# Kernel optimization log

Hardware: AMD Instinct MI355X
Metric: run time of the kernel (lower is better)

Reference implementation:

```python
import jax, jax.numpy as jnp
import numpy as np

N, T, D, C = 32, 512, 1024, 120
EPS = 1e-12
SCALE = 2.0 * (D ** 0.5)


def setup_inputs() -> dict:
    key = jax.random.key(0)
    ks = jax.random.split(key, 16)
    inp = {
        'anc_perm_input': jax.random.normal(ks[0], (N, T, D), dtype=jnp.float32),
        'pos_perm_input': jax.random.normal(ks[1], (N, T, D), dtype=jnp.float32),
        'neg_perm_input': jax.random.normal(ks[2], (N, T, D), dtype=jnp.float32),
        'anc_src_key_padding_mask': jax.random.randint(ks[3], (N, T), 0, 2) == 1,
        'pos_src_key_padding_mask': jax.random.randint(ks[4], (N, T), 0, 2) == 1,
        'neg_src_key_padding_mask': jax.random.randint(ks[5], (N, T), 0, 2) == 1,
        # learned parameters (stored as (in, out); math-equivalent to torch x @ W.T)
        'W_attn': jax.random.normal(ks[6], (D, D), dtype=jnp.float32) * 0.02,
        'b_attn': jnp.zeros((D,), dtype=jnp.float32),
        'W1': jax.random.normal(ks[7], (D, D), dtype=jnp.float32) * 0.02,
        'b1': jnp.zeros((D,), dtype=jnp.float32),
        'W2': jax.random.normal(ks[8], (D, D), dtype=jnp.float32) * 0.02,
        'b2': jnp.zeros((D,), dtype=jnp.float32),
        'ln_g': jnp.ones((D,), dtype=jnp.float32),
        'ln_b': jnp.zeros((D,), dtype=jnp.float32),
        'W_last': jax.random.normal(ks[9], (D, C), dtype=jnp.float32) * 0.02,
        'b_last': jnp.zeros((C,), dtype=jnp.float32),
    }
    return inp


def _ntd_nd(x, mask, W_attn, b_attn, W1, b1, W2, b2, ln_g, ln_b, W_last, b_last):
    # x: (N,T,D); mask: (N,T) bool, True = padding
    w = x @ W_attn + b_attn                                   # (N,T,D)
    valid = ~mask                                             # (N,T)
    scores = jnp.einsum('btd,bsd->bts', w, w)                 # (N,T,T)
    scores = jnp.where(valid[:, :, None] & valid[:, None, :], scores, 0.0)
    s = jnp.sum(scores, axis=1) / SCALE                       # (N,T)
    s = jnp.where(mask, -jnp.inf, s)
    attn = jax.nn.softmax(s, axis=1)                          # (N,T)
    # proj_head: duplicate OrderedDict key => linear1 -> relu -> linear2 (no final act)
    proj = jax.nn.relu(x @ W1 + b1) @ W2 + b2                 # (N,T,D)
    pooled = jnp.einsum('bt,btd->bd', attn, proj)             # (N,D)
    mu = jnp.mean(pooled, axis=-1, keepdims=True)
    var = jnp.var(pooled, axis=-1, keepdims=True)
    normed = (pooled - mu) / jnp.sqrt(var + EPS) * ln_g + ln_b
    return jax.nn.relu(normed) @ W_last + b_last              # (N,C)


def reference(anc_perm_input, pos_perm_input, neg_perm_input,
              anc_src_key_padding_mask, pos_src_key_padding_mask, neg_src_key_padding_mask,
              W_attn, b_attn, W1, b1, W2, b2, ln_g, ln_b, W_last, b_last):
    params = (W_attn, b_attn, W1, b1, W2, b2, ln_g, ln_b, W_last, b_last)
    anc = _ntd_nd(anc_perm_input, anc_src_key_padding_mask, *params)
    pos = _ntd_nd(pos_perm_input, pos_src_key_padding_mask, *params)
    neg = _ntd_nd(neg_perm_input, neg_src_key_padding_mask, *params)
    return (anc, pos, neg)
```

## Files before the change

kernel.cpp:

```cpp
#include <hip/hip_runtime.h>
#include <hip/hip_bf16.h>
#include <math.h>

#define N_B 32
#define T_S 512
#define D_D 1024
#define C_C 120
#define ZB 96
#define SCALE 64.0f

typedef unsigned short u16;
typedef __attribute__((ext_vector_type(8))) short short8;
typedef __attribute__((ext_vector_type(8))) unsigned short ushort8;
typedef __attribute__((ext_vector_type(4))) float floatx4;

__device__ inline u16 f2bf(float f) {
    union { __hip_bfloat16 h; u16 u; } c; c.h = __float2bfloat16(f); return c.u;
}
__device__ inline float bf2f(u16 u) {
    union { unsigned i; float f; } c; c.i = ((unsigned)u) << 16; return c.f;
}

__device__ inline void gll16(const void* g, void* l) {
    __builtin_amdgcn_global_load_lds((const __attribute__((address_space(1))) void*)g,
                                     (__attribute__((address_space(3))) void*)l,
                                     16, 0, 0);
}

__device__ inline bool mask_is_i8(const int* mk) {
    bool i8 = false;
#pragma unroll
    for (int i = 0; i < 16; i++) {
        unsigned v = ((const unsigned*)mk)[i];
        if (v > 1u) i8 = true;
    }
    return i8;
}
__device__ inline int mask_val(const int* mk, int idx, bool i8) {
    return i8 ? (int)((const signed char*)mk)[idx] : mk[idx];
}

__global__ __launch_bounds__(512)
void k_scan(const int* m0, const int* m1, const int* m2,
            int* __restrict__ slotbase, int* __restrict__ cnts,
            int* __restrict__ gb, int* __restrict__ zblk,
            int* __restrict__ mtot, u16* __restrict__ xp,
            float* __restrict__ attnw, float4* __restrict__ zreg) {
    int zb = blockIdx.x;
    int tid = threadIdx.x;
    {
        float4 zz4 = {0.f, 0.f, 0.f, 0.f};
        for (int i = zb * 512 + tid; i < (2 * 1024 * 1024 / 16); i += ZB * 512)
            zreg[i] = zz4;
    }
    bool i8_0 = mask_is_i8(m0), i8_1 = mask_is_i8(m1), i8_2 = mask_is_i8(m2);
    __shared__ unsigned short wc[ZB][8];
    __shared__ int scnt[ZB], sgb[ZB], stot;
    int wave = tid >> 6, lane = tid & 63;
#pragma unroll
    for (int it = 0; it < 12; it++) {
        int zb2 = wave * 12 + it;
        int z2 = zb2 >> 5, b2 = zb2 & 31;
        const int* mk = z2 == 0 ? m0 : (z2 == 1 ? m1 : m2);
        bool i8 = z2 == 0 ? i8_0 : (z2 == 1 ? i8_1 : i8_2);
        int c = 0;
        if (i8) {
            const signed char* p = (const signed char*)mk + b2 * T_S + lane * 8;
#pragma unroll
            for (int e = 0; e < 8; e++) c += (p[e] == 0);
        } else {
            const int* p = mk + b2 * T_S + lane * 8;
#pragma unroll
            for (int e = 0; e < 8; e++) c += (p[e] == 0);
        }
        c += __shfl_xor(c, 1, 64);
        c += __shfl_xor(c, 2, 64);
        c += __shfl_xor(c, 4, 64);
        if ((lane & 7) == 0) wc[zb2][lane >> 3] = (unsigned short)c;
    }
    __syncthreads();
    if (tid < ZB) {
        int s = 0;
#pragma unroll
        for (int c = 0; c < 8; c++) s += wc[tid][c];
        scnt[tid] = s;
    }
    __syncthreads();
    if (tid == 0) {
        int run = 0;
        for (int i = 0; i < ZB; i++) { sgb[i] = run; run += (scnt[i] + 63) & ~63; }
        stot = run;
    }
    __syncthreads();
    int cnt = scnt[zb], base = sgb[zb];
    if (tid == 0) {
        cnts[zb] = cnt; gb[zb] = base;
        int run = base;
#pragma unroll
        for (int c = 0; c < 8; c++) { slotbase[zb * 8 + c] = run; run += wc[zb][c]; }
        if (zb == ZB - 1) mtot[0] = stot;
    }
    int nb = (cnt + 63) >> 6;
    if (tid < nb) zblk[(base >> 6) + tid] = zb;
    int cend = (cnt + 63) & ~63;
    {
        u16* bp = xp + (size_t)(base + cnt) * D_D;
        int n8 = (cend - cnt) * (D_D / 8);
        ushort8 zz = {0,0,0,0,0,0,0,0};
        for (int i = tid; i < n8; i += 512)
            *(ushort8*)(bp + (size_t)i * 8) = zz;
    }
    if (zb == ZB - 1) {
        int tot = stot, tend = (tot + 255) & ~255;
        u16* bp = xp + (size_t)tot * D_D;
        int n8 = (tend - tot) * (D_D / 8);
        ushort8 zz = {0,0,0,0,0,0,0,0};
        for (int i = tid; i < n8; i += 512)
            *(ushort8*)(bp + (size_t)i * 8) = zz;
        for (int i = tid; i < tend - tot; i += 512) attnw[tot + i] = 0.f;
        if (tid < ((tend - tot) >> 6)) zblk[(tot >> 6) + tid] = 0;
    }
}

__global__ void k_prep(const float* __restrict__ W_attn, const float* __restrict__ W1,
                       const float* x0, const float* x1, const float* x2,
                       const int* m0, const int* m1, const int* m2,
                       const int* __restrict__ slotbase,
                       float* __restrict__ WT, u16* __restrict__ W1T,
                       float* __restrict__ xsum, u16* __restrict__ xp) {
    int bx = blockIdx.x;
    int tid = threadIdx.x;
    if (bx < 1024) {
        int tbx = bx & 31, tby = bx >> 5;
        __shared__ float tile[32][33];
        int tx = tid & 31, ty = tid >> 5;
#pragma unroll
        for (int j = 0; j < 32; j += 8)
            tile[ty + j][tx] = W_attn[(size_t)(tby*32 + ty + j)*D_D + tbx*32 + tx];
        __syncthreads();
#pragma unroll
        for (int j = 0; j < 32; j += 8)
            WT[(size_t)(tbx*32 + ty + j)*D_D + tby*32 + tx] = tile[tx][ty + j];
        __syncthreads();
#pragma unroll
        for (int j = 0; j < 32; j += 8)
            tile[ty + j][tx] = W1[(size_t)(tby*32 + ty + j)*D_D + tbx*32 + tx];
        __syncthreads();
#pragma unroll
        for (int j = 0; j < 32; j += 8)
            W1T[(size_t)(tbx*32 + ty + j)*D_D + tby*32 + tx] = f2bf(tile[tx][ty + j]);
        return;
    }
    int idx = bx - 1024;
    int chunk = idx & 7, zb = idx >> 3;
    int z = zb >> 5, b = zb & 31;
    const float* x = z == 0 ? x0 : (z == 1 ? x1 : x2);
    const int* mk = z == 0 ? m0 : (z == 1 ? m1 : m2);
    bool i8 = mask_is_i8(mk);
    int t0 = chunk * 64;
    __shared__ unsigned char s_list[64];
    __shared__ int s_cc;
    if (tid < 64) {
        bool v = (mask_val(mk, b * T_S + t0 + tid, i8) == 0);
        unsigned long long bal = __ballot(v);
        int pos = (int)__popcll(bal & ((1ull << tid) - 1ull));
        if (v) s_list[pos] = (unsigned char)tid;
        if (tid == 0) s_cc = (int)__popcll(bal);
    }
    __syncthreads();
    int cc = s_cc;
    int slot0 = slotbase[zb * 8 + chunk];
    const float4* xr = (const float4*)(x + (size_t)(b * T_S) * D_D);
    float4 acc = {0.f, 0.f, 0.f, 0.f};
#pragma unroll 4
    for (int j = 0; j < cc; j++) {
        int t = t0 + (int)s_list[j];
        float4 v = xr[(size_t)t * 256 + tid];
        union { __hip_bfloat162 h; ushort2 u; } c0, c1;
        c0.h = __float22bfloat162_rn({v.x, v.y});
        c1.h = __float22bfloat162_rn({v.z, v.w});
        ushort4 uu = {c0.u.x, c0.u.y, c1.u.x, c1.u.y};
        *(ushort4*)(xp + (size_t)(slot0 + j) * D_D + tid * 4) = uu;
        acc.x += v.x; acc.y += v.y; acc.z += v.z; acc.w += v.w;
    }
    float* xs = xsum + (size_t)zb * D_D + tid * 4;
    atomicAdd(xs + 0, acc.x); atomicAdd(xs + 1, acc.y);
    atomicAdd(xs + 2, acc.z); atomicAdd(xs + 3, acc.w);
}

__global__ void k_matvec(const float* __restrict__ W, const float* __restrict__ vin,
                         const float* __restrict__ bias, const int* __restrict__ bmul,
                         float scale, float* __restrict__ vout) {
    int z = blockIdx.z, bg = blockIdx.y;
    int och = blockIdx.x >> 3, kc = blockIdx.x & 7;
    int o = och * 256 + threadIdx.x;
    int brow = z * N_B + bg * 8;
    float acc[8] = {0.f, 0.f, 0.f, 0.f, 0.f, 0.f, 0.f, 0.f};
    if (kc == 0 && bias) {
        float bv = bias[o];
#pragma unroll
        for (int bb = 0; bb < 8; bb++)
            acc[bb] = bmul ? bv * (float)bmul[brow + bb] : bv;
    }
    const float* vi = vin + (size_t)brow * D_D + kc * 128;
    const float* Wp = W + (size_t)(kc * 128) * D_D + o;
#pragma unroll 4
    for (int i = 0; i < 128; i++) {
        float wv = Wp[(size_t)i * D_D];
#pragma unroll
        for (int bb = 0; bb < 8; bb++)
            acc[bb] += vi[(size_t)bb * D_D + i] * wv;
    }
#pragma unroll
    for (int bb = 0; bb < 8; bb++)
        atomicAdd(&vout[(size_t)(brow + bb) * D_D + o], acc[bb] * scale);
}

__global__ void k_dots(const u16* __restrict__ xp, const float* __restrict__ vs,
                       const int* __restrict__ zblk, const int* __restrict__ mtot,
                       float* __restrict__ sdot) {
    int t0 = blockIdx.x * 4;
    if (t0 >= mtot[0]) return;
    int t = t0 + (threadIdx.x >> 6);
    int lane = threadIdx.x & 63;
    int zb = zblk[t0 >> 6];
    const u16* xr = xp + (size_t)t * D_D;
    const float* vr = vs + (size_t)zb * D_D;
    float acc = 0.f;
#pragma unroll
    for (int i = 0; i < 2; i++) {
        short8 v = *(const short8*)(xr + i * 512 + lane * 8);
        const float* vp = vr + i * 512 + lane * 8;
        float4 a0 = *(const float4*)(vp);
        float4 a1 = *(const float4*)(vp + 4);
        acc += bf2f((u16)v[0]) * a0.x + bf2f((u16)v[1]) * a0.y
             + bf2f((u16)v[2]) * a0.z + bf2f((u16)v[3]) * a0.w
             + bf2f((u16)v[4]) * a1.x + bf2f((u16)v[5]) * a1.y
             + bf2f((u16)v[6]) * a1.z + bf2f((u16)v[7]) * a1.w;
    }
#pragma unroll
    for (int off = 32; off; off >>= 1) acc += __shfl_xor(acc, off, 64);
    if (lane == 0) sdot[t] = acc;
}

__global__ void k_smax(const float* __restrict__ sdot, const int* __restrict__ cnts,
                       const int* __restrict__ gb, float* __restrict__ attnw) {
    int zb = blockIdx.x, tid = threadIdx.x;
    __shared__ float redm[8], reds[8];
    int cnt = cnts[zb], base = gb[zb];
    int wave = tid >> 6, lane = tid & 63;
    float v = (tid < cnt) ? sdot[base + tid] : -INFINITY;
    float mx = v;
#pragma unroll
    for (int off = 32; off; off >>= 1) mx = fmaxf(mx, __shfl_xor(mx, off, 64));
    if (lane == 0) redm[wave] = mx;
    __syncthreads();
    mx = redm[0];
#pragma unroll
    for (int k = 1; k < 8; k++) mx = fmaxf(mx, redm[k]);
    float e = __expf(v - mx);
    float es = e;
#pragma unroll
    for (int off = 32; off; off >>= 1) es += __shfl_xor(es, off, 64);
    if (lane == 0) reds[wave] = es;
    __syncthreads();
    float tot = 0.f;
#pragma unroll
    for (int k = 0; k < 8; k++) tot += reds[k];
    int cend = (cnt + 63) & ~63;
    if (tid < cend) attnw[base + tid] = (tid < cnt) ? (e / tot) : 0.f;
}

#define STAGE_TILE(buf, k0)                                                   \
    {                                                                         \
        _Pragma("unroll")                                                     \
        for (int i_ = 0; i_ < 4; i_++) {                                      \
            int r0_ = i_ * 64 + wave * 8;                                     \
            int rr_ = r0_ + srow;                                             \
            int gc_ = cp ^ srow;            \
            gll16(abase + (size_t)rr_ * D_D + (k0) + gc_ * 8,                 \
                  &As[buf][r0_ * 64]);                                        \
            gll16(bbase + (size_t)rr_ * D_D + (k0) + gc_ * 8,                 \
                  &Bs[buf][r0_ * 64]);                                        \
        }                                                                     \
    }

__global__ __launch_bounds__(512, 1)
void k_gemm_bf16(const u16* __restrict__ xp, const u16* __restrict__ W1T,
                 const float* __restrict__ b1, const float* __restrict__ attnw,
                 const int* __restrict__ zblk, const int* __restrict__ mtot,
                 float* __restrict__ rbuf) {
    int bid = blockIdx.x;
    int sub = bid & 31;
    int Mt = (bid >> 5) * 8 + (sub & 7);
    int Nt = sub >> 3;
    int row0 = Mt * 256, N0 = Nt * 256;
    if (row0 >= mtot[0]) return;

    __shared__ __align__(16) u16 As[2][256 * 64];
    __shared__ __align__(16) u16 Bs[2][256 * 64];
    __shared__ float sAttn[256];
    int tid = threadIdx.x;
    int wave = tid >> 6, lane = tid & 63;
    if (tid < 256) sAttn[tid] = attnw[row0 + tid];

    int wy = wave >> 2, wx = wave & 3;
    int q = lane >> 4, cidx = lane & 15;
    int srow = lane >> 3;
    int cp = lane & 7;

    floatx4 acc[8][4];
#pragma unroll
    for (int mi = 0; mi < 8; mi++)
#pragma unroll
        for (int ni = 0; ni < 4; ni++)
            acc[mi][ni] = (floatx4){0.f, 0.f, 0.f, 0.f};

    const u16* abase = xp + (size_t)row0 * D_D;
    const u16* bbase = W1T + (size_t)N0 * D_D;

    STAGE_TILE(0, 0)
    __syncthreads();
    int cur = 0;
#pragma unroll 2
    for (int kt = 0; kt < 16; kt++) {
        if (kt < 15) { STAGE_TILE(cur ^ 1, (kt + 1) << 6) }
        __builtin_amdgcn_sched_barrier(0);
#pragma unroll
        for (int ks = 0; ks < 2; ks++) {
            short8 a[8], bfr[4];
#pragma unroll
            for (int mi = 0; mi < 8; mi++) {
                int m = wy * 128 + mi * 16 + cidx;
                a[mi] = *(const short8*)&As[cur][m * 64 + ((((ks << 2) | q) ^ (m & 7)) << 3)];
            }
#pragma unroll
            for (int ni = 0; ni < 4; ni++) {
                int n = wx * 64 + ni * 16 + cidx;
                bfr[ni] = *(const short8*)&Bs[cur][n * 64 + ((((ks << 2) | q) ^ (n & 7)) << 3)];
            }
#pragma unroll
            for (int mi = 0; mi < 8; mi++)
#pragma unroll
                for (int ni = 0; ni < 4; ni++)
                    acc[mi][ni] = __builtin_amdgcn_mfma_f32_16x16x32_bf16(
                        a[mi], bfr[ni], acc[mi][ni], 0, 0, 0);
        }
        __syncthreads();
        cur ^= 1;
    }

    int zb0 = zblk[(row0 >> 6) + wy * 2];
    int zb1 = zblk[(row0 >> 6) + wy * 2 + 1];
#pragma unroll
    for (int ni = 0; ni < 4; ni++) {
        int ng = N0 + wx * 64 + ni * 16 + cidx;
        float b1v = b1[ng];
        float s0 = 0.f, s1 = 0.f;
#pragma unroll
        for (int mi = 0; mi < 8; mi++) {
            float part = 0.f;
#pragma unroll
            for (int rg = 0; rg < 4; rg++) {
                int ml = wy * 128 + mi * 16 + q * 4 + rg;
                float hv = fmaxf(acc[mi][ni][rg] + b1v, 0.f);
                part += hv * sAttn[ml];
            }
            if (mi < 4) s0 += part; else s1 += part;
        }
        s0 += __shfl_xor(s0, 16, 64); s0 += __shfl_xor(s0, 32, 64);
        s1 += __shfl_xor(s1, 16, 64); s1 += __shfl_xor(s1, 32, 64);
        if (lane < 16) {
            atomicAdd(&rbuf[(size_t)zb0 * D_D + ng], s0);
            atomicAdd(&rbuf[(size_t)zb1 * D_D + ng], s1);
        }
    }
}

__global__ void k_fin(const float* __restrict__ pooled, const float* __restrict__ ln_g,
                      const float* __restrict__ ln_b, const float* __restrict__ Wl,
                      const float* __restrict__ bl, float* __restrict__ out) {
    int zb = blockIdx.x;
    int tid = threadIdx.x;
    __shared__ float nr[D_D];
    __shared__ float redA[8], redB[8];
    __shared__ float ps[4][C_C];
    const float* p = pooled + (size_t)zb * D_D;
    int o0 = tid, o1 = tid + 512;
    float a0 = p[o0], a1 = p[o1];
    float s1 = a0 + a1, s2 = a0 * a0 + a1 * a1;
#pragma unroll
    for (int off = 32; off; off >>= 1) {
        s1 += __shfl_xor(s1, off, 64);
        s2 += __shfl_xor(s2, off, 64);
    }
    int w = tid >> 6;
    if ((tid & 63) == 0) { redA[w] = s1; redB[w] = s2; }
    __syncthreads();
    float t1 = 0.f, t2 = 0.f;
#pragma unroll
    for (int k = 0; k < 8; k++) { t1 += redA[k]; t2 += redB[k]; }
    float mu = t1 * (1.0f / D_D);
    float var = t2 * (1.0f / D_D) - mu * mu;
    float rstd = 1.0f / sqrtf(var + 1e-12f);
    nr[o0] = fmaxf((a0 - mu) * rstd * ln_g[o0] + ln_b[o0], 0.f);
    nr[o1] = fmaxf((a1 - mu) * rstd * ln_g[o1] + ln_b[o1], 0.f);
    __syncthreads();
    if (tid < 4 * C_C) {
        int seg = tid / C_C, c = tid - seg * C_C;
        const float* wp = Wl + (size_t)(seg * 256) * C_C + c;
        const float* np = nr + seg * 256;
        float acc = 0.f;
#pragma unroll 8
        for (int d = 0; d < 256; d++)
            acc += np[d] * wp[(size_t)d * C_C];
        ps[seg][c] = acc;
    }
    __syncthreads();
    if (tid < C_C)
        out[(size_t)zb * C_C + tid] =
            bl[tid] + ps[0][tid] + ps[1][tid] + ps[2][tid] + ps[3][tid];
}

extern "C" void kernel_launch(void* const* d_in, const int* in_sizes, int n_in,
                              void* d_out, int out_size, void* d_ws, size_t ws_size,
                              hipStream_t stream) {
    const float* x0 = (const float*)d_in[0];
    const float* x1 = (const float*)d_in[1];
    const float* x2 = (const float*)d_in[2];
    const int* m0 = (const int*)d_in[3];
    const int* m1 = (const int*)d_in[4];
    const int* m2 = (const int*)d_in[5];
    const float* W_attn = (const float*)d_in[6];
    const float* b_attn = (const float*)d_in[7];
    const float* W1 = (const float*)d_in[8];
    const float* b1 = (const float*)d_in[9];
    const float* W2 = (const float*)d_in[10];
    const float* b2 = (const float*)d_in[11];
    const float* ln_g = (const float*)d_in[12];
    const float* ln_b = (const float*)d_in[13];
    const float* W_last = (const float*)d_in[14];
    const float* b_last = (const float*)d_in[15];
    float* out = (float*)d_out;

    char* wsb = (char*)d_ws;
    const size_t MB = 1 << 20;
    float* WT     = (float*)(wsb);
    u16*   W1T    = (u16*)  (wsb + 4 * MB);
    float* xsum   = (float*)(wsb + 6 * MB);
    float* rbuf   = (float*)(wsb + 6 * MB + 393216);
    float* wsum   = (float*)(wsb + 6 * MB + 786432);
    float* vs     = (float*)(wsb + 6 * MB + 1179648);
    float* pooled = (float*)(wsb + 6 * MB + 1572864);
    float* sdot   = (float*)(wsb + 8 * MB);
    float* attnw  = (float*)(wsb + 8 * MB + 262144);
    int*   slotb  = (int*)  (wsb + 8 * MB + 524288);
    int*   cnts   = (int*)  (wsb + 8 * MB + 528384);
    int*   gb     = (int*)  (wsb + 8 * MB + 532480);
    int*   mtot   = (int*)  (wsb + 8 * MB + 536576);
    int*   zblk   = (int*)  (wsb + 8 * MB + 540672);
    u16*   xp     = (u16*)  (wsb + 9 * MB);

    k_scan  <<<ZB, 512, 0, stream>>>(m0, m1, m2, slotb, cnts, gb, zblk, mtot,
                                     xp, attnw, (float4*)(wsb + 6 * MB));
    k_prep  <<<1792, 256, 0, stream>>>(W_attn, W1, x0, x1, x2, m0, m1, m2,
                                       slotb, WT, W1T, xsum, xp);
    k_matvec<<<dim3(32, 4, 3), 256, 0, stream>>>(W_attn, xsum, b_attn, cnts, 1.0f, wsum);
    k_matvec<<<dim3(32, 4, 3), 256, 0, stream>>>(WT, wsum, nullptr, nullptr, 1.0f / SCALE, vs);
    k_dots  <<<12288, 256, 0, stream>>>(xp, vs, zblk, mtot, sdot);
    k_smax  <<<ZB, 512, 0, stream>>>(sdot, cnts, gb, attnw);
    k_gemm_bf16<<<768, 512, 0, stream>>>(xp, W1T, b1, attnw, zblk, mtot, rbuf);
    k_matvec<<<dim3(32, 4, 3), 256, 0, stream>>>(W2, rbuf, b2, nullptr, 1.0f, pooled);
    k_fin   <<<ZB, 512, 0, stream>>>(pooled, ln_g, ln_b, W_last, b_last, out);
}
```

Measured before the change: 373.3 us.

## Fuse softmax into GEMM prologue and weight transposes into scan kernel

Removes the separate softmax kernel: each GEMM block recomputes the per-sequence max and sum from the dot scores for the sequences its 256 rows touch, then builds its attention weights in shared memory. Moves the W_attn/W1 transpose blocks from the prep kernel into the scan kernel, which now launches 1024 extra blocks, so the prep kernel only packs x. This cuts two kernel launches' worth of serialization and the attnw round trip. In exchange every GEMM block repeats softmax reductions with extra barriers, and padded tail rows now depend on zblk and sdot values instead of explicitly zeroed attnw.

```diff
diff --git a/kernel.cpp b/kernel.cpp
--- a/kernel.cpp
+++ b/kernel.cpp
@@ -42,12 +42,36 @@
 
 __global__ __launch_bounds__(512)
 void k_scan(const int* m0, const int* m1, const int* m2,
+            const float* __restrict__ W_attn, const float* __restrict__ W1,
             int* __restrict__ slotbase, int* __restrict__ cnts,
             int* __restrict__ gb, int* __restrict__ zblk,
             int* __restrict__ mtot, u16* __restrict__ xp,
-            float* __restrict__ attnw, float4* __restrict__ zreg) {
+            float* __restrict__ WT, u16* __restrict__ W1T,
+            float4* __restrict__ zreg) {
     int zb = blockIdx.x;
     int tid = threadIdx.x;
+    if (zb >= ZB) {
+        int bx = zb - ZB;
+        int tbx = bx & 31, tby = bx >> 5;
+        __shared__ float tile[32][33];
+        int tx = tid & 31, ty = tid >> 5;
+#pragma unroll
+        for (int j = 0; j < 32; j += 16)
+            tile[ty + j][tx] = W_attn[(size_t)(tby*32 + ty + j)*D_D + tbx*32 + tx];
+        __syncthreads();
+#pragma unroll
+        for (int j = 0; j < 32; j += 16)
+            WT[(size_t)(tbx*32 + ty + j)*D_D + tby*32 + tx] = tile[tx][ty + j];
+        __syncthreads();
+#pragma unroll
+        for (int j = 0; j < 32; j += 16)
+            tile[ty + j][tx] = W1[(size_t)(tby*32 + ty + j)*D_D + tbx*32 + tx];
+        __syncthreads();
+#pragma unroll
+        for (int j = 0; j < 32; j += 16)
+            W1T[(size_t)(tbx*32 + ty + j)*D_D + tby*32 + tx] = f2bf(tile[tx][ty + j]);
+        return;
+    }
     {
         float4 zz4 = {0.f, 0.f, 0.f, 0.f};
         for (int i = zb * 512 + tid; i < (2 * 1024 * 1024 / 16); i += ZB * 512)
@@ -117,41 +141,16 @@
         ushort8 zz = {0,0,0,0,0,0,0,0};
         for (int i = tid; i < n8; i += 512)
             *(ushort8*)(bp + (size_t)i * 8) = zz;
-        for (int i = tid; i < tend - tot; i += 512) attnw[tot + i] = 0.f;
         if (tid < ((tend - tot) >> 6)) zblk[(tot >> 6) + tid] = 0;
     }
 }
 
-__global__ void k_prep(const float* __restrict__ W_attn, const float* __restrict__ W1,
-                       const float* x0, const float* x1, const float* x2,
+__global__ void k_prep(const float* x0, const float* x1, const float* x2,
                        const int* m0, const int* m1, const int* m2,
                        const int* __restrict__ slotbase,
-                       float* __restrict__ WT, u16* __restrict__ W1T,
                        float* __restrict__ xsum, u16* __restrict__ xp) {
-    int bx = blockIdx.x;
+    int idx = blockIdx.x;
     int tid = threadIdx.x;
-    if (bx < 1024) {
-        int tbx = bx & 31, tby = bx >> 5;
-        __shared__ float tile[32][33];
-        int tx = tid & 31, ty = tid >> 5;
-#pragma unroll
-        for (int j = 0; j < 32; j += 8)
-            tile[ty + j][tx] = W_attn[(size_t)(tby*32 + ty + j)*D_D + tbx*32 + tx];
-        __syncthreads();
-#pragma unroll
-        for (int j = 0; j < 32; j += 8)
-            WT[(size_t)(tbx*32 + ty + j)*D_D + tby*32 + tx] = tile[tx][ty + j];
-        __syncthreads();
-#pragma unroll
-        for (int j = 0; j < 32; j += 8)
-            tile[ty + j][tx] = W1[(size_t)(tby*32 + ty + j)*D_D + tbx*32 + tx];
-        __syncthreads();
-#pragma unroll
-        for (int j = 0; j < 32; j += 8)
-            W1T[(size_t)(tbx*32 + ty + j)*D_D + tby*32 + tx] = f2bf(tile[tx][ty + j]);
-        return;
-    }
-    int idx = bx - 1024;
     int chunk = idx & 7, zb = idx >> 3;
     int z = zb >> 5, b = zb & 31;
     const float* x = z == 0 ? x0 : (z == 1 ? x1 : x2);
@@ -243,34 +242,6 @@
     if (lane == 0) sdot[t] = acc;
 }
 
-__global__ void k_smax(const float* __restrict__ sdot, const int* __restrict__ cnts,
-                       const int* __restrict__ gb, float* __restrict__ attnw) {
-    int zb = blockIdx.x, tid = threadIdx.x;
-    __shared__ float redm[8], reds[8];
-    int cnt = cnts[zb], base = gb[zb];
-    int wave = tid >> 6, lane = tid & 63;
-    float v = (tid < cnt) ? sdot[base + tid] : -INFINITY;
-    float mx = v;
-#pragma unroll
-    for (int off = 32; off; off >>= 1) mx = fmaxf(mx, __shfl_xor(mx, off, 64));
-    if (lane == 0) redm[wave] = mx;
-    __syncthreads();
-    mx = redm[0];
-#pragma unroll
-    for (int k = 1; k < 8; k++) mx = fmaxf(mx, redm[k]);
-    float e = __expf(v - mx);
-    float es = e;
-#pragma unroll
-    for (int off = 32; off; off >>= 1) es += __shfl_xor(es, off, 64);
-    if (lane == 0) reds[wave] = es;
-    __syncthreads();
-    float tot = 0.f;
-#pragma unroll
-    for (int k = 0; k < 8; k++) tot += reds[k];
-    int cend = (cnt + 63) & ~63;
-    if (tid < cend) attnw[base + tid] = (tid < cnt) ? (e / tot) : 0.f;
-}
-
 #define STAGE_TILE(buf, k0)                                                   \
     {                                                                         \
         _Pragma("unroll")                                                     \
@@ -287,7 +258,8 @@
 
 __global__ __launch_bounds__(512, 1)
 void k_gemm_bf16(const u16* __restrict__ xp, const u16* __restrict__ W1T,
-                 const float* __restrict__ b1, const float* __restrict__ attnw,
+                 const float* __restrict__ b1, const float* __restrict__ sdot,
+                 const int* __restrict__ cnts, const int* __restrict__ gb,
                  const int* __restrict__ zblk, const int* __restrict__ mtot,
                  float* __restrict__ rbuf) {
     int bid = blockIdx.x;
@@ -300,9 +272,48 @@
     __shared__ __align__(16) u16 As[2][256 * 64];
     __shared__ __align__(16) u16 Bs[2][256 * 64];
     __shared__ float sAttn[256];
+    __shared__ float redm[8], reds[8];
     int tid = threadIdx.x;
     int wave = tid >> 6, lane = tid & 63;
-    if (tid < 256) sAttn[tid] = attnw[row0 + tid];
+
+    {
+        int g0 = row0 >> 6;
+        int prevzb = -1, czb_cnt = 0, czb_base = 0;
+        float mx = 0.f, tot = 1.f;
+#pragma unroll
+        for (int g = 0; g < 4; g++) {
+            int zbg = zblk[g0 + g];
+            if (zbg != prevzb) {
+                czb_cnt = cnts[zbg]; czb_base = gb[zbg];
+                float v = (tid < czb_cnt) ? sdot[czb_base + tid] : -INFINITY;
+                float m = v;
+#pragma unroll
+                for (int off = 32; off; off >>= 1) m = fmaxf(m, __shfl_xor(m, off, 64));
+                if (lane == 0) redm[wave] = m;
+                __syncthreads();
+                m = redm[0];
+#pragma unroll
+                for (int k = 1; k < 8; k++) m = fmaxf(m, redm[k]);
+                float e = __expf(v - m);
+#pragma unroll
+                for (int off = 32; off; off >>= 1) e += __shfl_xor(e, off, 64);
+                if (lane == 0) reds[wave] = e;
+                __syncthreads();
+                float t_ = 0.f;
+#pragma unroll
+                for (int k = 0; k < 8; k++) t_ += reds[k];
+                mx = m; tot = t_; prevzb = zbg;
+            }
+            if (tid < 64) {
+                int row = row0 + g * 64 + tid;
+                int tl = row - czb_base;
+                float w = 0.f;
+                if (tl < czb_cnt) w = __expf(sdot[row] - mx) / tot;
+                sAttn[g * 64 + tid] = w;
+            }
+            __syncthreads();
+        }
+    }
 
     int wy = wave >> 2, wx = wave & 3;
     int q = lane >> 4, cidx = lane & 15;
@@ -453,7 +464,6 @@
     float* vs     = (float*)(wsb + 6 * MB + 1179648);
     float* pooled = (float*)(wsb + 6 * MB + 1572864);
     float* sdot   = (float*)(wsb + 8 * MB);
-    float* attnw  = (float*)(wsb + 8 * MB + 262144);
     int*   slotb  = (int*)  (wsb + 8 * MB + 524288);
     int*   cnts   = (int*)  (wsb + 8 * MB + 528384);
     int*   gb     = (int*)  (wsb + 8 * MB + 532480);
@@ -461,15 +471,14 @@
     int*   zblk   = (int*)  (wsb + 8 * MB + 540672);
     u16*   xp     = (u16*)  (wsb + 9 * MB);
 
-    k_scan  <<<ZB, 512, 0, stream>>>(m0, m1, m2, slotb, cnts, gb, zblk, mtot,
-                                     xp, attnw, (float4*)(wsb + 6 * MB));
-    k_prep  <<<1792, 256, 0, stream>>>(W_attn, W1, x0, x1, x2, m0, m1, m2,
-                                       slotb, WT, W1T, xsum, xp);
+    k_scan  <<<ZB + 1024, 512, 0, stream>>>(m0, m1, m2, W_attn, W1,
+                                            slotb, cnts, gb, zblk, mtot,
+                                            xp, WT, W1T, (float4*)(wsb + 6 * MB));
+    k_prep  <<<768, 256, 0, stream>>>(x0, x1, x2, m0, m1, m2, slotb, xsum, xp);
     k_matvec<<<dim3(32, 4, 3), 256, 0, stream>>>(W_attn, xsum, b_attn, cnts, 1.0f, wsum);
     k_matvec<<<dim3(32, 4, 3), 256, 0, stream>>>(WT, wsum, nullptr, nullptr, 1.0f / SCALE, vs);
     k_dots  <<<12288, 256, 0, stream>>>(xp, vs, zblk, mtot, sdot);
-    k_smax  <<<ZB, 512, 0, stream>>>(sdot, cnts, gb, attnw);
-    k_gemm_bf16<<<768, 512, 0, stream>>>(xp, W1T, b1, attnw, zblk, mtot, rbuf);
+    k_gemm_bf16<<<768, 512, 0, stream>>>(xp, W1T, b1, sdot, cnts, gb, zblk, mtot, rbuf);
     k_matvec<<<dim3(32, 4, 3), 256, 0, stream>>>(W2, rbuf, b2, nullptr, 1.0f, pooled);
     k_fin   <<<ZB, 512, 0, stream>>>(pooled, ln_g, ln_b, W_last, b_last, out);
 }
```

Result: no change. 375.6 us (+0.6%).
